# Optimization experiments

Hardware: AMD Instinct MI355X
Metric: run time of the kernel (lower is better)

## Reference

```python
import jax, jax.numpy as jnp
import numpy as np

CAPACITY = 0.5

def setup_inputs() -> dict:
    key = jax.random.key(0)
    kx, kw = jax.random.split(key)
    b, s, d = 4, 4096, 2048
    x = jax.random.normal(kx, (b, s, d), dtype=jnp.float32)
    # nn.Linear(d_model, 1, bias=False) weight: [1, d_model] -> store as [d_model]
    gate_w = jax.random.normal(kw, (d,), dtype=jnp.float32) * (1.0 / np.sqrt(d))
    return {"x": x, "gate_w": gate_w}

def reference(x, gate_w):
    b, s, _ = x.shape
    logits = jnp.einsum('bsd,d->bs', x, gate_w)            # [b, s]
    weights = jax.nn.sigmoid(logits.astype(jnp.float32)).astype(x.dtype)[..., None]  # [b, s, 1]
    num_selected = max(1, int(s * CAPACITY))
    if num_selected >= s:
        mask = jnp.ones_like(weights)
    else:
        _, top_idx = jax.lax.top_k(logits, num_selected)    # [b, k]
        mask2d = jnp.zeros((b, s), dtype=x.dtype).at[jnp.arange(b)[:, None], top_idx].set(1.0)
        mask = mask2d[..., None]                            # [b, s, 1]
    aux_loss = jnp.var(weights, ddof=1)                     # torch var is unbiased
    return mask, weights, aux_loss
```

## Files before the change

kernel.cpp:

```cpp
#include <hip/hip_runtime.h>
#include <hip/hip_bf16.h>

#define BATCH 4
#define SEQ   4096
#define DMODEL 2048
#define KSEL  2048

__global__ __launch_bounds__(256) void logits_kernel(
    const float* __restrict__ x,
    const float* __restrict__ gate_w,
    float* __restrict__ logits,
    float* __restrict__ weights)
{
    const int wave = threadIdx.x >> 6;
    const int lane = threadIdx.x & 63;
    const int wid  = blockIdx.x * 4 + wave;
    const int row0 = wid * 2;

    const float4* wr = reinterpret_cast<const float4*>(gate_w);
    float4 wv[8];
#pragma unroll
    for (int t = 0; t < 8; ++t) wv[t] = wr[t * 64 + lane];

    double rsum[2];
#pragma unroll
    for (int r = 0; r < 2; ++r) {
        const float4* xr =
            reinterpret_cast<const float4*>(x + (size_t)(row0 + r) * DMODEL);
        float4 xv[8];
#pragma unroll
        for (int t = 0; t < 8; ++t) xv[t] = xr[t * 64 + lane];

        double a0 = 0.0, a1 = 0.0, a2 = 0.0, a3 = 0.0;
#pragma unroll
        for (int t = 0; t < 8; ++t) {
            a0 += (double)xv[t].x * (double)wv[t].x;
            a1 += (double)xv[t].y * (double)wv[t].y;
            a2 += (double)xv[t].z * (double)wv[t].z;
            a3 += (double)xv[t].w * (double)wv[t].w;
        }
        rsum[r] = (a0 + a1) + (a2 + a3);
    }

#pragma unroll
    for (int off = 32; off > 0; off >>= 1) {
        rsum[0] += __shfl_down(rsum[0], off, 64);
        rsum[1] += __shfl_down(rsum[1], off, 64);
    }

    if (lane == 0) {
#pragma unroll
        for (int r = 0; r < 2; ++r) {
            float l = (float)rsum[r];
            logits[row0 + r]  = l;
            weights[row0 + r] = 1.0f / (1.0f + expf(-l));
        }
    }
}

__global__ __launch_bounds__(512) void select_finalize_kernel(
    const float* __restrict__ logits,
    const float* __restrict__ weights,
    float* __restrict__ mask,
    float* __restrict__ aux)
{
    if (blockIdx.x == BATCH * 64) {
        const int n = BATCH * SEQ;
        double s = 0.0, s2 = 0.0;
        for (int i = threadIdx.x; i < n; i += 512) {
            double w = (double)weights[i];
            s  += w;
            s2 += w * w;
        }
#pragma unroll
        for (int off = 32; off > 0; off >>= 1) {
            s  += __shfl_down(s,  off, 64);
            s2 += __shfl_down(s2, off, 64);
        }
        __shared__ double sh[16];
        const int wid  = threadIdx.x >> 6;
        const int lane = threadIdx.x & 63;
        if (lane == 0) { sh[wid] = s; sh[wid + 8] = s2; }
        __syncthreads();
        if (threadIdx.x == 0) {
            double S = 0.0, S2 = 0.0;
#pragma unroll
            for (int w = 0; w < 8; ++w) { S += sh[w]; S2 += sh[w + 8]; }
            double mean = S / n;
            double var  = (S2 - (double)n * mean * mean) / (double)(n - 1);
            *aux = (float)var;
        }
        return;
    }

    const int b    = blockIdx.x >> 6;
    const int eblk = blockIdx.x & 63;

    __shared__ float L[SEQ];
    __shared__ int sh_gt[64][9];
    __shared__ int sh_eq[64][9];

    const float* row = logits + b * SEQ;
    for (int i = threadIdx.x; i < SEQ / 4; i += 512)
        reinterpret_cast<float4*>(L)[i] =
            reinterpret_cast<const float4*>(row)[i];
    __syncthreads();

    const int e     = threadIdx.x & 63;
    const int slice = threadIdx.x >> 6;
    const int i     = eblk * 64 + e;
    const float v   = L[i];

    int gt = 0, eq = 0;
    const int j0 = slice * (SEQ / 8);
#pragma unroll 4
    for (int j = j0; j < j0 + SEQ / 8; j += 4) {
        float4 q = *reinterpret_cast<const float4*>(&L[j]);
        gt += (q.x > v) + (q.y > v) + (q.z > v) + (q.w > v);
        eq += (q.x == v) + (q.y == v) + (q.z == v) + (q.w == v);
    }
    sh_gt[e][slice] = gt;
    sh_eq[e][slice] = eq;
    __syncthreads();

    if (slice == 0) {
        int GT = 0, EQ = 0;
#pragma unroll
        for (int t = 0; t < 8; ++t) { GT += sh_gt[e][t]; EQ += sh_eq[e][t]; }
        float m;
        if (GT >= KSEL) {
            m = 0.0f;
        } else if (EQ == 1) {
            m = 1.0f;
        } else {
            int lower = 0;
            for (int j = 0; j < i; ++j) lower += (L[j] == v);
            m = (GT + lower < KSEL) ? 1.0f : 0.0f;
        }
        mask[b * SEQ + i] = m;
    }
}

extern "C" void kernel_launch(void* const* d_in, const int* in_sizes, int n_in,
                              void* d_out, int out_size, void* d_ws, size_t ws_size,
                              hipStream_t stream) {
    const float* x      = (const float*)d_in[0];
    const float* gate_w = (const float*)d_in[1];

    float* out     = (float*)d_out;
    float* mask    = out;
    float* weights = out + BATCH * SEQ;
    float* aux     = out + 2 * BATCH * SEQ;

    float* logits = (float*)d_ws;

    logits_kernel<<<dim3(BATCH * SEQ / 8), dim3(256), 0, stream>>>(
        x, gate_w, logits, weights);

    select_finalize_kernel<<<dim3(BATCH * 64 + 1), dim3(512), 0, stream>>>(
        logits, weights, mask, aux);
}
```

Measured before the change: 39.29 us.

## Use grid-stride logits kernel and finer-grained rank-count selection blocks

The logits kernel now launches a fixed grid of 1024 blocks and loops over row pairs with a grid-stride loop, so gate weights are loaded once per wave and reused across rows. The selection kernel is split into 1024 blocks of 256 threads: each block ranks 16 elements using 16 slices, and each slice starts its scan at a staggered offset to avoid LDS bank conflicts. This spreads the rank counting across more CUs. The cost is that every block reloads the full 16KB logits row into LDS, which is 4x more redundant global reads.

```diff
diff --git a/kernel.cpp b/kernel.cpp
--- a/kernel.cpp
+++ b/kernel.cpp
@@ -12,62 +12,65 @@
     float* __restrict__ logits,
     float* __restrict__ weights)
 {
-    const int wave = threadIdx.x >> 6;
-    const int lane = threadIdx.x & 63;
-    const int wid  = blockIdx.x * 4 + wave;
-    const int row0 = wid * 2;
+    const int wave   = threadIdx.x >> 6;
+    const int lane   = threadIdx.x & 63;
+    const int nwaves = gridDim.x * 4;
 
     const float4* wr = reinterpret_cast<const float4*>(gate_w);
     float4 wv[8];
 #pragma unroll
     for (int t = 0; t < 8; ++t) wv[t] = wr[t * 64 + lane];
 
-    double rsum[2];
+    for (int wid = blockIdx.x * 4 + wave; wid < (BATCH * SEQ) / 2; wid += nwaves) {
+        const int row0 = wid * 2;
+
+        double rsum[2];
 #pragma unroll
-    for (int r = 0; r < 2; ++r) {
-        const float4* xr =
-            reinterpret_cast<const float4*>(x + (size_t)(row0 + r) * DMODEL);
-        float4 xv[8];
+        for (int r = 0; r < 2; ++r) {
+            const float4* xr =
+                reinterpret_cast<const float4*>(x + (size_t)(row0 + r) * DMODEL);
+            float4 xv[8];
 #pragma unroll
-        for (int t = 0; t < 8; ++t) xv[t] = xr[t * 64 + lane];
+            for (int t = 0; t < 8; ++t) xv[t] = xr[t * 64 + lane];
 
-        double a0 = 0.0, a1 = 0.0, a2 = 0.0, a3 = 0.0;
+            double a0 = 0.0, a1 = 0.0, a2 = 0.0, a3 = 0.0;
 #pragma unroll
-        for (int t = 0; t < 8; ++t) {
-            a0 += (double)xv[t].x * (double)wv[t].x;
-            a1 += (double)xv[t].y * (double)wv[t].y;
-            a2 += (double)xv[t].z * (double)wv[t].z;
-            a3 += (double)xv[t].w * (double)wv[t].w;
+            for (int t = 0; t < 8; ++t) {
+                a0 += (double)xv[t].x * (double)wv[t].x;
+                a1 += (double)xv[t].y * (double)wv[t].y;
+                a2 += (double)xv[t].z * (double)wv[t].z;
+                a3 += (double)xv[t].w * (double)wv[t].w;
+            }
+            rsum[r] = (a0 + a1) + (a2 + a3);
         }
-        rsum[r] = (a0 + a1) + (a2 + a3);
-    }
 
 #pragma unroll
-    for (int off = 32; off > 0; off >>= 1) {
-        rsum[0] += __shfl_down(rsum[0], off, 64);
-        rsum[1] += __shfl_down(rsum[1], off, 64);
-    }
+        for (int off = 32; off > 0; off >>= 1) {
+            rsum[0] += __shfl_down(rsum[0], off, 64);
+            rsum[1] += __shfl_down(rsum[1], off, 64);
+        }
 
-    if (lane == 0) {
+        if (lane == 0) {
 #pragma unroll
-        for (int r = 0; r < 2; ++r) {
-            float l = (float)rsum[r];
-            logits[row0 + r]  = l;
-            weights[row0 + r] = 1.0f / (1.0f + expf(-l));
+            for (int r = 0; r < 2; ++r) {
+                float l = (float)rsum[r];
+                logits[row0 + r]  = l;
+                weights[row0 + r] = 1.0f / (1.0f + expf(-l));
+            }
         }
     }
 }
 
-__global__ __launch_bounds__(512) void select_finalize_kernel(
+__global__ __launch_bounds__(256) void select_finalize_kernel(
     const float* __restrict__ logits,
     const float* __restrict__ weights,
     float* __restrict__ mask,
     float* __restrict__ aux)
 {
-    if (blockIdx.x == BATCH * 64) {
+    if (blockIdx.x == 1024) {
         const int n = BATCH * SEQ;
         double s = 0.0, s2 = 0.0;
-        for (int i = threadIdx.x; i < n; i += 512) {
+        for (int i = threadIdx.x; i < n; i += 256) {
             double w = (double)weights[i];
             s  += w;
             s2 += w * w;
@@ -77,15 +80,14 @@
             s  += __shfl_down(s,  off, 64);
             s2 += __shfl_down(s2, off, 64);
         }
-        __shared__ double sh[16];
+        __shared__ double sh[8];
         const int wid  = threadIdx.x >> 6;
         const int lane = threadIdx.x & 63;
-        if (lane == 0) { sh[wid] = s; sh[wid + 8] = s2; }
+        if (lane == 0) { sh[wid] = s; sh[wid + 4] = s2; }
         __syncthreads();
         if (threadIdx.x == 0) {
-            double S = 0.0, S2 = 0.0;
-#pragma unroll
-            for (int w = 0; w < 8; ++w) { S += sh[w]; S2 += sh[w + 8]; }
+            double S  = sh[0] + sh[1] + sh[2] + sh[3];
+            double S2 = sh[4] + sh[5] + sh[6] + sh[7];
             double mean = S / n;
             double var  = (S2 - (double)n * mean * mean) / (double)(n - 1);
             *aux = (float)var;
@@ -93,31 +95,34 @@
         return;
     }
 
-    const int b    = blockIdx.x >> 6;
-    const int eblk = blockIdx.x & 63;
+    const int blk   = blockIdx.x;
+    const int chunk = blk >> 2;
+    const int b     = chunk >> 6;
+    const int q     = blk & 3;
 
     __shared__ float L[SEQ];
-    __shared__ int sh_gt[64][9];
-    __shared__ int sh_eq[64][9];
+    __shared__ int sh_gt[16][17];
+    __shared__ int sh_eq[16][17];
 
     const float* row = logits + b * SEQ;
-    for (int i = threadIdx.x; i < SEQ / 4; i += 512)
+    for (int i = threadIdx.x; i < SEQ / 4; i += 256)
         reinterpret_cast<float4*>(L)[i] =
             reinterpret_cast<const float4*>(row)[i];
     __syncthreads();
 
-    const int e     = threadIdx.x & 63;
-    const int slice = threadIdx.x >> 6;
-    const int i     = eblk * 64 + e;
+    const int e     = threadIdx.x & 15;
+    const int slice = threadIdx.x >> 4;
+    const int i     = (chunk & 63) * 64 + q * 16 + e;
     const float v   = L[i];
 
     int gt = 0, eq = 0;
-    const int j0 = slice * (SEQ / 8);
+    const int j0 = slice * (SEQ / 16);
 #pragma unroll 4
-    for (int j = j0; j < j0 + SEQ / 8; j += 4) {
-        float4 q = *reinterpret_cast<const float4*>(&L[j]);
-        gt += (q.x > v) + (q.y > v) + (q.z > v) + (q.w > v);
-        eq += (q.x == v) + (q.y == v) + (q.z == v) + (q.w == v);
+    for (int tt = 0; tt < 64; ++tt) {
+        const int t = (tt + slice) & 63;
+        float4 qd = *reinterpret_cast<const float4*>(&L[j0 + t * 4]);
+        gt += (qd.x > v) + (qd.y > v) + (qd.z > v) + (qd.w > v);
+        eq += (qd.x == v) + (qd.y == v) + (qd.z == v) + (qd.w == v);
     }
     sh_gt[e][slice] = gt;
     sh_eq[e][slice] = eq;
@@ -126,7 +131,7 @@
     if (slice == 0) {
         int GT = 0, EQ = 0;
 #pragma unroll
-        for (int t = 0; t < 8; ++t) { GT += sh_gt[e][t]; EQ += sh_eq[e][t]; }
+        for (int s = 0; s < 16; ++s) { GT += sh_gt[e][s]; EQ += sh_eq[e][s]; }
         float m;
         if (GT >= KSEL) {
             m = 0.0f;
@@ -154,9 +159,9 @@
 
     float* logits = (float*)d_ws;
 
-    logits_kernel<<<dim3(BATCH * SEQ / 8), dim3(256), 0, stream>>>(
+    logits_kernel<<<dim3(1024), dim3(256), 0, stream>>>(
         x, gate_w, logits, weights);
 
-    select_finalize_kernel<<<dim3(BATCH * 64 + 1), dim3(512), 0, stream>>>(
+    select_finalize_kernel<<<dim3(1025), dim3(256), 0, stream>>>(
         logits, weights, mask, aux);
 }
```

Result: slower. 50.51 us (+28.5%).
